# Kernel optimization log

Measured on AMD Instinct MI355X. Metric: run time of the kernel, lower is better.

The kernel has to match this reference:

```python
import jax, jax.numpy as jnp
import numpy as np

N_QUBITS = 8
N_LAYERS = 2


def _apply_1q(state, U, wire):
    # state: (B, 2, ..., 2) with N_QUBITS qubit axes; U: (2,2) complex, shared over batch
    s = jnp.moveaxis(state, 1 + wire, 1)
    shp = s.shape
    out = jnp.einsum('ij,bjr->bir', U, s.reshape(shp[0], 2, -1)).reshape(shp)
    return jnp.moveaxis(out, 1, 1 + wire)


def _apply_cnot(state, c, t):
    s = jnp.moveaxis(state, (1 + c, 1 + t), (1, 2))  # (B, ctrl, tgt, ...)
    s_new = jnp.stack([s[:, 0], jnp.flip(s[:, 1], axis=1)], axis=1)
    return jnp.moveaxis(s_new, (1, 2), (1 + c, 1 + t))


def _circuit(angles, q_weights):
    # angles: (B, N) real; q_weights: (L, N, 3) real
    B = angles.shape[0]
    N = N_QUBITS
    # AngleEmbedding with RY on |0...0> -> product state [cos(a/2), sin(a/2)] per qubit
    half = angles * 0.5
    state = jnp.ones((B, 1), dtype=jnp.complex64)
    for i in range(N):
        v = jnp.stack([jnp.cos(half[:, i]), jnp.sin(half[:, i])], axis=-1).astype(jnp.complex64)
        state = (state[:, :, None] * v[:, None, :]).reshape(B, -1)
    state = state.reshape((B,) + (2,) * N)
    # StronglyEntanglingLayers: per layer, Rot(phi,theta,omega) on each wire then CNOT ring
    L = q_weights.shape[0]
    for l in range(L):
        for i in range(N):
            phi = q_weights[l, i, 0]
            theta = q_weights[l, i, 1]
            omega = q_weights[l, i, 2]
            c = jnp.cos(theta * 0.5).astype(jnp.complex64)
            s_ = jnp.sin(theta * 0.5).astype(jnp.complex64)
            ep = jnp.exp(-0.5j * (phi + omega).astype(jnp.complex64))
            em = jnp.exp(-0.5j * (phi - omega).astype(jnp.complex64))
            # Rot = RZ(omega) RY(theta) RZ(phi)
            U = jnp.stack([jnp.stack([ep * c, -jnp.conj(em) * s_]),
                           jnp.stack([em * s_, jnp.conj(ep) * c])])
            state = _apply_1q(state, U, i)
        r = l % (N - 1) + 1  # default range pattern of StronglyEntanglingLayers
        for i in range(N):
            state = _apply_cnot(state, i, (i + r) % N)
    # <Z_i> = P(bit_i=0) - P(bit_i=1)
    probs = jnp.real(state * jnp.conj(state))
    zs = []
    for i in range(N):
        pm = jnp.moveaxis(probs, 1 + i, 1).reshape(B, 2, -1).sum(-1)
        zs.append(pm[:, 0] - pm[:, 1])
    return jnp.stack(zs, axis=-1)  # (B, N) real


def setup_inputs() -> dict:
    key = jax.random.key(0)
    k1, k2, k3, k4 = jax.random.split(key, 4)
    B = 32768
    pca_x = jax.random.normal(k1, (B, N_QUBITS), dtype=jnp.float32)
    q_weights = jax.random.uniform(k2, (N_LAYERS, N_QUBITS, 3), dtype=jnp.float32) * (2.0 * np.pi)
    W = jax.random.normal(k3, (N_QUBITS, 64), dtype=jnp.float32) * 0.35
    b = jax.random.normal(k4, (64,), dtype=jnp.float32) * 0.02
    gamma = jnp.ones((64,), dtype=jnp.float32)
    beta = jnp.zeros((64,), dtype=jnp.float32)
    return {"pca_x": pca_x, "q_weights": q_weights, "W": W, "b": b, "gamma": gamma, "beta": beta}


def reference(pca_x, q_weights, W, b, gamma, beta):
    angles = jax.nn.sigmoid(pca_x) * jnp.pi  # (B, 8)
    z = _circuit(angles, q_weights).astype(pca_x.dtype)  # (B, 8) PauliZ expvals
    h = z @ W + b  # (B, 64)
    mu = jnp.mean(h, axis=-1, keepdims=True)
    var = jnp.mean((h - mu) ** 2, axis=-1, keepdims=True)
    hn = (h - mu) / jnp.sqrt(var + 1e-5) * gamma + beta
    return jax.nn.gelu(hn, approximate=False)
```

## Files before the change

### kernel.cpp

```cpp
#include <hip/hip_runtime.h>
#include <math.h>

#define DEVFN __device__ __forceinline__

typedef __attribute__((ext_vector_type(8))) _Float16 f16x8;
typedef __attribute__((ext_vector_type(4))) float f32x4;

DEVFN float shxor(float v, int m) { return __shfl_xor(v, m, 64); }

template<int W>
DEVFN void rot_gate(int lane, float (&sr)[4], float (&si)[4], const float* u) {
  const float u00r=u[0], u00i=u[1], u01r=u[2], u01i=u[3];
  const float u10r=u[4], u10i=u[5], u11r=u[6], u11i=u[7];
  if constexpr (W <= 5) {
    constexpr int M = 1 << (5 - W);
    const bool hi = (lane & M) != 0;
    const float cmr = hi ? u11r : u00r, cmi = hi ? u11i : u00i;
    const float cor = hi ? u10r : u01r, coi = hi ? u10i : u01i;
    #pragma unroll
    for (int k = 0; k < 4; ++k) {
      float orr = shxor(sr[k], M);
      float oii = shxor(si[k], M);
      float nr = cmr*sr[k] - cmi*si[k] + cor*orr - coi*oii;
      float ni = cmr*si[k] + cmi*sr[k] + cor*oii + coi*orr;
      sr[k] = nr; si[k] = ni;
    }
  } else {
    constexpr int KB = (W == 6) ? 2 : 1;
    #pragma unroll
    for (int k0 = 0; k0 < 4; ++k0) {
      if ((k0 & KB) == 0) {
        const int k1 = k0 | KB;
        float ar = sr[k0], ai = si[k0];
        float br = sr[k1], bi = si[k1];
        sr[k0] = u00r*ar - u00i*ai + u01r*br - u01i*bi;
        si[k0] = u00r*ai + u00i*ar + u01r*bi + u01i*br;
        sr[k1] = u10r*ar - u10i*ai + u11r*br - u11i*bi;
        si[k1] = u10r*ai + u10i*ar + u11r*bi + u11i*br;
      }
    }
  }
}

template<int C, int T>
DEVFN void cnot_gate(int lane, float (&sr)[4], float (&si)[4]) {
  constexpr int PC = 7 - C, PT = 7 - T;
  if constexpr (PT >= 2) {
    constexpr int M = 1 << (PT - 2);
    #pragma unroll
    for (int k = 0; k < 4; ++k) {
      float orr = shxor(sr[k], M);
      float oii = shxor(si[k], M);
      bool ctrl;
      if constexpr (PC >= 2) ctrl = ((lane >> (PC - 2)) & 1) != 0;
      else                   ctrl = ((k >> PC) & 1) != 0;
      if (ctrl) { sr[k] = orr; si[k] = oii; }
    }
  } else {
    float tr[4], ti[4];
    #pragma unroll
    for (int k = 0; k < 4; ++k) { tr[k] = sr[k]; ti[k] = si[k]; }
    #pragma unroll
    for (int k = 0; k < 4; ++k) {
      bool ctrl;
      if constexpr (PC >= 2) ctrl = ((lane >> (PC - 2)) & 1) != 0;
      else                   ctrl = ((k >> PC) & 1) != 0;
      if (ctrl) { sr[k] = tr[k ^ (1 << PT)]; si[k] = ti[k ^ (1 << PT)]; }
    }
  }
}

__global__ __launch_bounds__(64) void qsb_prep(
    const float* __restrict__ qw, const float* __restrict__ Wm,
    const float* __restrict__ bias,
    _Float16* __restrict__ Bfrag, float* __restrict__ stats) {
  __shared__ float uL[16 * 8];
  int bid = blockIdx.x;
  int lane = threadIdx.x;
  if (bid < 256) {
    if (lane < 16) {
      int l = lane >> 3, i = lane & 7;
      float phi = qw[l*24 + i*3 + 0];
      float th  = qw[l*24 + i*3 + 1];
      float om  = qw[l*24 + i*3 + 2];
      float cth = cosf(0.5f*th), sth = sinf(0.5f*th);
      float ap = 0.5f*(phi+om), am = 0.5f*(phi-om);
      float cap = cosf(ap), sap = sinf(ap);
      float cam = cosf(am), sam = sinf(am);
      float* u = &uL[lane*8];
      u[0] =  cap*cth; u[1] = -sap*cth;
      u[2] = -cam*sth; u[3] = -sam*sth;
      u[4] =  cam*sth; u[5] = -sam*sth;
      u[6] =  cap*cth; u[7] =  sap*cth;
    }
    __syncthreads();
    int col = bid;
    float sr[4], si[4];
    #pragma unroll
    for (int k = 0; k < 4; ++k) { sr[k] = (lane*4 + k == col) ? 1.f : 0.f; si[k] = 0.f; }
    rot_gate<0>(lane, sr, si, &uL[0*8]);
    rot_gate<1>(lane, sr, si, &uL[1*8]);
    rot_gate<2>(lane, sr, si, &uL[2*8]);
    rot_gate<3>(lane, sr, si, &uL[3*8]);
    rot_gate<4>(lane, sr, si, &uL[4*8]);
    rot_gate<5>(lane, sr, si, &uL[5*8]);
    rot_gate<6>(lane, sr, si, &uL[6*8]);
    rot_gate<7>(lane, sr, si, &uL[7*8]);
    cnot_gate<0,1>(lane, sr, si);
    cnot_gate<1,2>(lane, sr, si);
    cnot_gate<2,3>(lane, sr, si);
    cnot_gate<3,4>(lane, sr, si);
    cnot_gate<4,5>(lane, sr, si);
    cnot_gate<5,6>(lane, sr, si);
    cnot_gate<6,7>(lane, sr, si);
    cnot_gate<7,0>(lane, sr, si);
    rot_gate<0>(lane, sr, si, &uL[(8+0)*8]);
    rot_gate<1>(lane, sr, si, &uL[(8+1)*8]);
    rot_gate<2>(lane, sr, si, &uL[(8+2)*8]);
    rot_gate<3>(lane, sr, si, &uL[(8+3)*8]);
    rot_gate<4>(lane, sr, si, &uL[(8+4)*8]);
    rot_gate<5>(lane, sr, si, &uL[(8+5)*8]);
    rot_gate<6>(lane, sr, si, &uL[(8+6)*8]);
    rot_gate<7>(lane, sr, si, &uL[(8+7)*8]);
    cnot_gate<0,2>(lane, sr, si);
    cnot_gate<1,3>(lane, sr, si);
    cnot_gate<2,4>(lane, sr, si);
    cnot_gate<3,5>(lane, sr, si);
    cnot_gate<4,6>(lane, sr, si);
    cnot_gate<5,7>(lane, sr, si);
    cnot_gate<6,0>(lane, sr, si);
    cnot_gate<7,1>(lane, sr, si);
    const int ks = col >> 5, kg = (col >> 3) & 3, e = col & 7;
    #pragma unroll
    for (int k = 0; k < 4; ++k) {
      int a = lane*4 + k;
      int ch = a >> 5, nf = (a >> 4) & 1, cf = a & 15;
      int pos = (kg*16 + cf)*8 + e;
      Bfrag[((ch*4 + nf    )*8 + ks)*512 + pos] = (_Float16)sr[k];
      Bfrag[((ch*4 + 2 + nf)*8 + ks)*512 + pos] = (_Float16)si[k];
    }
  } else {
    int t = lane;
    {
      int i = t >> 3, j = t & 7;
      float s = 0.f;
      for (int c = 0; c < 64; ++c) s += Wm[i*64 + c] * Wm[j*64 + c];
      stats[16 + t] = s * 0.015625f;
    }
    if (t < 8) {
      float s = 0.f, sb = 0.f;
      for (int c = 0; c < 64; ++c) { float w = Wm[t*64 + c]; s += w; sb += w * bias[c]; }
      stats[t]     = s * 0.015625f;
      stats[8 + t] = 2.f * sb * 0.015625f;
    }
    if (t == 0) {
      float s = 0.f, s2 = 0.f;
      for (int c = 0; c < 64; ++c) { s += bias[c]; s2 += bias[c]*bias[c]; }
      stats[80] = s * 0.015625f;
      stats[81] = s2 * 0.015625f;
    }
  }
}

__global__ __launch_bounds__(512, 4) void qsb_main(
    const float* __restrict__ pca, const _Float16* __restrict__ Bfrag,
    const float* __restrict__ statsG,
    const float* __restrict__ Wm, const float* __restrict__ bias,
    const float* __restrict__ gamma, const float* __restrict__ beta,
    float* __restrict__ out, int B) {
  __shared__ __align__(16) _Float16 A3[16384];
  __shared__ float zpart[64 * 49];
  __shared__ float zrow[64 * 8];
  __shared__ float musig[64 * 2];
  __shared__ float Wl[512];
  __shared__ float biasL[64], gammaL[64], betaL[64];
  __shared__ float statsL[82];

  const int tid = threadIdx.x;
  const int wid = tid >> 6, lane = tid & 63;
  const int r0 = blockIdx.x * 64;

  Wl[tid] = Wm[tid];
  if (tid < 64) { biasL[tid] = bias[tid]; gammaL[tid] = gamma[tid]; betaL[tid] = beta[tid]; }
  if (tid >= 64 && tid < 146) statsL[tid - 64] = statsG[tid - 64];

  {
    const int rl = tid >> 3, tq = tid & 7;
    const int r = r0 + rl;
    float cv[8], sv[8];
    #pragma unroll
    for (int w = 0; w < 8; ++w) { cv[w] = 1.f; sv[w] = 0.f; }
    if (r < B) {
      #pragma unroll
      for (int w = 0; w < 8; ++w) {
        float x = pca[r*8 + w];
        float sg = __builtin_amdgcn_rcpf(1.f + __expf(-x));
        float ang = 1.5707963267948966f * sg;
        cv[w] = __cosf(ang); sv[w] = __sinf(ang);
      }
    }
    float base = ((tq & 4) ? sv[0] : cv[0]) * ((tq & 2) ? sv[1] : cv[1])
               * ((tq & 1) ? sv[2] : cv[2]);
    float arr[32];
    arr[0] = base;
    #pragma unroll
    for (int p = 0; p < 5; ++p) {
      const int w = 7 - p;
      const int sz = 1 << p;
      #pragma unroll
      for (int i = 0; i < (1 << p); ++i) {
        arr[i + sz] = arr[i] * sv[w];
        arr[i]      = arr[i] * cv[w];
      }
    }
    _Float16* dstBase = &A3[((tq*4 + (rl >> 4))*16 + (rl & 15))*32];
    #pragma unroll
    for (int ib = 0; ib < 4; ++ib) {
      f16x8 v;
      #pragma unroll
      for (int j = 0; j < 8; ++j) v[j] = (_Float16)arr[ib*8 + j];
      *(f16x8*)(dstBase + (ib ^ (tq & 3))*8) = v;
    }
  }
  __syncthreads();

  const int cfrag = lane & 15, kgrp = lane >> 4;
  f32x4 acc[4][4];
  #pragma unroll
  for (int m = 0; m < 4; ++m)
    #pragma unroll
    for (int q = 0; q < 4; ++q) acc[m][q] = (f32x4){0.f, 0.f, 0.f, 0.f};

  const _Float16* Bw = Bfrag + (wid*4)*8*512 + lane*8;
  #pragma unroll 2
  for (int ks = 0; ks < 8; ++ks) {
    const int slot = (kgrp ^ (ks & 3))*8;
    f16x8 af[4];
    #pragma unroll
    for (int m = 0; m < 4; ++m)
      af[m] = *(const f16x8*)&A3[((ks*4 + m)*16 + cfrag)*32 + slot];
    #pragma unroll
    for (int q = 0; q < 4; ++q) {
      f16x8 bq = *(const f16x8*)(Bw + (q*8 + ks)*512);
      #pragma unroll
      for (int m = 0; m < 4; ++m)
        acc[m][q] = __builtin_amdgcn_mfma_f32_16x16x32_f16(af[m], bq, acc[m][q], 0, 0, 0);
    }
  }

  #pragma unroll
  for (int m = 0; m < 4; ++m) {
    #pragma unroll
    for (int j = 0; j < 4; ++j) {
      float re0 = acc[m][0][j], re1 = acc[m][1][j];
      float im0 = acc[m][2][j], im1 = acc[m][3][j];
      float p0 = re0*re0 + im0*im0;
      float p1 = re1*re1 + im1*im1;
      float T = p0 + p1, S4 = p0 - p1;
      #pragma unroll
      for (int mm = 1; mm < 16; mm <<= 1) {
        S4 += shxor(S4, mm);
        float t2 = shxor(T, mm);
        T = (lane & mm) ? (t2 - T) : (T + t2);
      }
      const int row = m*16 + kgrp*4 + j;
      float* zp = &zpart[row*49 + wid*6];
      const int cc = lane & 15;
      if      (cc == 0) { zp[0] = T; zp[1] = S4; }
      else if (cc == 8) zp[2] = T;
      else if (cc == 4) zp[3] = T;
      else if (cc == 2) zp[4] = T;
      else if (cc == 1) zp[5] = T;
    }
  }
  __syncthreads();

  {
    const int row = tid >> 3, wire = tid & 7;
    const float* zp = &zpart[row*49];
    const int slot = (wire < 3) ? 0 : (wire - 2);
    const int sm = (wire == 0) ? 4 : (wire == 1) ? 2 : (wire == 2) ? 1 : 0;
    float a = 0.f;
    #pragma unroll
    for (int ch = 0; ch < 8; ++ch) {
      float v = zp[ch*6 + slot];
      a += (ch & sm) ? -v : v;
    }
    zrow[row*8 + wire] = a;
  }
  __syncthreads();

  {
    const int row = tid >> 3, ii = tid & 7;
    float zj[8];
    #pragma unroll
    for (int j = 0; j < 8; ++j) zj[j] = zrow[row*8 + j];
    float qi = statsL[8 + ii];
    #pragma unroll
    for (int j = 0; j < 8; ++j) qi += statsL[16 + ii*8 + j] * zj[j];
    float e2p = zj[ii] * qi;
    float mup = statsL[ii] * zj[ii];
    e2p += shxor(e2p, 1); e2p += shxor(e2p, 2); e2p += shxor(e2p, 4);
    mup += shxor(mup, 1); mup += shxor(mup, 2); mup += shxor(mup, 4);
    if (ii == 0) {
      float mu = mup + statsL[80];
      float e2 = e2p + statsL[81];
      float var = e2 - mu*mu;
      musig[row*2]     = mu;
      musig[row*2 + 1] = rsqrtf(fmaxf(var, 0.f) + 1e-5f);
    }
  }
  __syncthreads();

  #pragma unroll
  for (int rr = 0; rr < 8; ++rr) {
    const int row = wid*8 + rr;
    const int gr = r0 + row;
    float h = biasL[lane];
    #pragma unroll
    for (int i = 0; i < 8; ++i) h = fmaf(zrow[row*8 + i], Wl[i*64 + lane], h);
    float hn = (h - musig[row*2]) * musig[row*2 + 1] * gammaL[lane] + betaL[lane];
    float ge = 0.5f * hn * (1.f + erff(hn * 0.70710678118654752f));
    if (gr < B) out[gr*64 + lane] = ge;
  }
}

extern "C" void kernel_launch(void* const* d_in, const int* in_sizes, int n_in,
                              void* d_out, int out_size, void* d_ws, size_t ws_size,
                              hipStream_t stream) {
  const float* pca   = (const float*)d_in[0];
  const float* qw    = (const float*)d_in[1];
  const float* Wm    = (const float*)d_in[2];
  const float* bias  = (const float*)d_in[3];
  const float* gamma = (const float*)d_in[4];
  const float* beta  = (const float*)d_in[5];
  float* out = (float*)d_out;

  _Float16* Bfrag = (_Float16*)d_ws;
  float* stats = (float*)((char*)d_ws + 512*256*2);

  int B = in_sizes[0] / 8;

  hipLaunchKernelGGL(qsb_prep, dim3(257), dim3(64), 0, stream, qw, Wm, bias, Bfrag, stats);
  int blocks = (B + 63) / 64;
  hipLaunchKernelGGL(qsb_main, dim3(blocks), dim3(512), 0, stream,
                     pca, Bfrag, stats, Wm, bias, gamma, beta, out, B);
}
```

Measured before the change: 31.42 us.

## Halve block size and reduce Pauli-Z probabilities with a sign-matrix MFMA

Blocks now cover 32 rows with 256 threads, and each wave handles two 16-wide chunks of the state. Per-chunk B fragments are double-buffered in registers so loads overlap the MFMAs. The shuffle-based butterfly that computed the Z expectation sums is replaced by writing squared amplitudes to LDS as fp16 and multiplying them by a constant ±1 sign fragment with one MFMA. The z-combine and stats stages are merged, and one block barrier is dropped because each wave only reads its own rows. This cuts shuffle and ALU work and raises occupancy, but rounding probabilities to fp16 before summing adds precision risk.

```diff
diff --git a/kernel.cpp b/kernel.cpp
--- a/kernel.cpp
+++ b/kernel.cpp
@@ -162,27 +162,47 @@
   }
 }
 
-__global__ __launch_bounds__(512, 4) void qsb_main(
+__global__ __launch_bounds__(256, 4) void qsb_main(
     const float* __restrict__ pca, const _Float16* __restrict__ Bfrag,
     const float* __restrict__ statsG,
     const float* __restrict__ Wm, const float* __restrict__ bias,
     const float* __restrict__ gamma, const float* __restrict__ beta,
     float* __restrict__ out, int B) {
-  __shared__ __align__(16) _Float16 A3[16384];
-  __shared__ float zpart[64 * 49];
-  __shared__ float zrow[64 * 8];
-  __shared__ float musig[64 * 2];
+  __shared__ __align__(16) _Float16 A3[8192];
+  __shared__ __align__(16) _Float16 YL[4 * 1280];
+  __shared__ float zpart[2304];
+  __shared__ float zrow[256];
+  __shared__ float musig[64];
   __shared__ float Wl[512];
   __shared__ float biasL[64], gammaL[64], betaL[64];
   __shared__ float statsL[82];
 
   const int tid = threadIdx.x;
   const int wid = tid >> 6, lane = tid & 63;
-  const int r0 = blockIdx.x * 64;
-
-  Wl[tid] = Wm[tid];
-  if (tid < 64) { biasL[tid] = bias[tid]; gammaL[tid] = gamma[tid]; betaL[tid] = beta[tid]; }
-  if (tid >= 64 && tid < 146) statsL[tid - 64] = statsG[tid - 64];
+  const int cfrag = lane & 15, kgrp = lane >> 4;
+  const int r0 = blockIdx.x * 32;
+
+  #pragma unroll
+  for (int i = tid; i < 512; i += 256) Wl[i] = Wm[i];
+  if (tid >= 256 - 64) {
+    int t = tid - (256 - 64);
+    biasL[t] = bias[t]; gammaL[t] = gamma[t]; betaL[t] = beta[t];
+  }
+  if (tid < 82) statsL[tid] = statsG[tid];
+
+  f16x8 sfrag;
+  #pragma unroll
+  for (int e = 0; e < 8; ++e) {
+    float v;
+    if      (cfrag == 0) v = 1.f;
+    else if (cfrag == 1) v = (kgrp & 2) ? -1.f : 1.f;
+    else if (cfrag == 2) v = (kgrp & 1) ? -1.f : 1.f;
+    else if (cfrag == 3) v = (e & 4)    ? -1.f : 1.f;
+    else if (cfrag == 4) v = (e & 2)    ? -1.f : 1.f;
+    else if (cfrag == 5) v = (e & 1)    ? -1.f : 1.f;
+    else v = 0.f;
+    sfrag[e] = (_Float16)v;
+  }
 
   {
     const int rl = tid >> 3, tq = tid & 7;
@@ -213,7 +233,7 @@
         arr[i]      = arr[i] * cv[w];
       }
     }
-    _Float16* dstBase = &A3[((tq*4 + (rl >> 4))*16 + (rl & 15))*32];
+    _Float16* dstBase = &A3[((tq*2 + (rl >> 4))*16 + (rl & 15))*32];
     #pragma unroll
     for (int ib = 0; ib < 4; ++ib) {
       f16x8 v;
@@ -224,85 +244,98 @@
   }
   __syncthreads();
 
-  const int cfrag = lane & 15, kgrp = lane >> 4;
-  f32x4 acc[4][4];
+  _Float16* Yw = &YL[wid * 1280];
   #pragma unroll
-  for (int m = 0; m < 4; ++m)
-    #pragma unroll
-    for (int q = 0; q < 4; ++q) acc[m][q] = (f32x4){0.f, 0.f, 0.f, 0.f};
-
-  const _Float16* Bw = Bfrag + (wid*4)*8*512 + lane*8;
-  #pragma unroll 2
-  for (int ks = 0; ks < 8; ++ks) {
-    const int slot = (kgrp ^ (ks & 3))*8;
-    f16x8 af[4];
-    #pragma unroll
-    for (int m = 0; m < 4; ++m)
-      af[m] = *(const f16x8*)&A3[((ks*4 + m)*16 + cfrag)*32 + slot];
-    #pragma unroll
-    for (int q = 0; q < 4; ++q) {
-      f16x8 bq = *(const f16x8*)(Bw + (q*8 + ks)*512);
-      #pragma unroll
-      for (int m = 0; m < 4; ++m)
-        acc[m][q] = __builtin_amdgcn_mfma_f32_16x16x32_f16(af[m], bq, acc[m][q], 0, 0, 0);
-    }
-  }
-
-  #pragma unroll
-  for (int m = 0; m < 4; ++m) {
-    #pragma unroll
-    for (int j = 0; j < 4; ++j) {
-      float re0 = acc[m][0][j], re1 = acc[m][1][j];
-      float im0 = acc[m][2][j], im1 = acc[m][3][j];
-      float p0 = re0*re0 + im0*im0;
-      float p1 = re1*re1 + im1*im1;
-      float T = p0 + p1, S4 = p0 - p1;
-      #pragma unroll
-      for (int mm = 1; mm < 16; mm <<= 1) {
-        S4 += shxor(S4, mm);
-        float t2 = shxor(T, mm);
-        T = (lane & mm) ? (t2 - T) : (T + t2);
-      }
-      const int row = m*16 + kgrp*4 + j;
-      float* zp = &zpart[row*49 + wid*6];
-      const int cc = lane & 15;
-      if      (cc == 0) { zp[0] = T; zp[1] = S4; }
-      else if (cc == 8) zp[2] = T;
-      else if (cc == 4) zp[3] = T;
-      else if (cc == 2) zp[4] = T;
-      else if (cc == 1) zp[5] = T;
+  for (int c = 0; c < 2; ++c) {
+    const int ch = wid*2 + c;
+    const _Float16* Bw = Bfrag + (size_t)(ch*4)*8*512 + lane*8;
+
+    f32x4 acc[2][4];
+    #pragma unroll
+    for (int m = 0; m < 2; ++m)
+      #pragma unroll
+      for (int q = 0; q < 4; ++q) acc[m][q] = (f32x4){0.f, 0.f, 0.f, 0.f};
+
+    f16x8 bqA[4], bqB[4];
+    #pragma unroll
+    for (int q = 0; q < 4; ++q) bqA[q] = *(const f16x8*)(Bw + (q*8 + 0)*512);
+
+    #pragma unroll
+    for (int kp = 0; kp < 4; ++kp) {
+      const int ks0 = kp*2, ks1 = kp*2 + 1;
+      #pragma unroll
+      for (int q = 0; q < 4; ++q) bqB[q] = *(const f16x8*)(Bw + (q*8 + ks1)*512);
+      {
+        f16x8 af0 = *(const f16x8*)&A3[((ks0*2 + 0)*16 + cfrag)*32 + (kgrp ^ (ks0 & 3))*8];
+        f16x8 af1 = *(const f16x8*)&A3[((ks0*2 + 1)*16 + cfrag)*32 + (kgrp ^ (ks0 & 3))*8];
+        #pragma unroll
+        for (int q = 0; q < 4; ++q) {
+          acc[0][q] = __builtin_amdgcn_mfma_f32_16x16x32_f16(af0, bqA[q], acc[0][q], 0, 0, 0);
+          acc[1][q] = __builtin_amdgcn_mfma_f32_16x16x32_f16(af1, bqA[q], acc[1][q], 0, 0, 0);
+        }
+      }
+      if (kp < 3) {
+        #pragma unroll
+        for (int q = 0; q < 4; ++q) bqA[q] = *(const f16x8*)(Bw + (q*8 + ks0 + 2)*512);
+      }
+      {
+        f16x8 af0 = *(const f16x8*)&A3[((ks1*2 + 0)*16 + cfrag)*32 + (kgrp ^ (ks1 & 3))*8];
+        f16x8 af1 = *(const f16x8*)&A3[((ks1*2 + 1)*16 + cfrag)*32 + (kgrp ^ (ks1 & 3))*8];
+        #pragma unroll
+        for (int q = 0; q < 4; ++q) {
+          acc[0][q] = __builtin_amdgcn_mfma_f32_16x16x32_f16(af0, bqB[q], acc[0][q], 0, 0, 0);
+          acc[1][q] = __builtin_amdgcn_mfma_f32_16x16x32_f16(af1, bqB[q], acc[1][q], 0, 0, 0);
+        }
+      }
+    }
+
+    #pragma unroll
+    for (int m = 0; m < 2; ++m) {
+      #pragma unroll
+      for (int nf = 0; nf < 2; ++nf) {
+        #pragma unroll
+        for (int j = 0; j < 4; ++j) {
+          float re = acc[m][nf][j], im = acc[m][2 + nf][j];
+          float p = re*re + im*im;
+          Yw[m*640 + (kgrp*4 + j)*40 + nf*16 + cfrag] = (_Float16)p;
+        }
+      }
+    }
+    #pragma unroll
+    for (int m = 0; m < 2; ++m) {
+      f16x8 yfrag = *(const f16x8*)&Yw[m*640 + (lane & 15)*40 + kgrp*8];
+      f32x4 d = __builtin_amdgcn_mfma_f32_16x16x32_f16(yfrag, sfrag, (f32x4){0.f,0.f,0.f,0.f}, 0, 0, 0);
+      if (cfrag < 6) {
+        #pragma unroll
+        for (int j = 0; j < 4; ++j)
+          zpart[(ch*32 + m*16 + kgrp*4 + j)*9 + cfrag] = d[j];
+      }
     }
   }
   __syncthreads();
 
   {
-    const int row = tid >> 3, wire = tid & 7;
-    const float* zp = &zpart[row*49];
-    const int slot = (wire < 3) ? 0 : (wire - 2);
-    const int sm = (wire == 0) ? 4 : (wire == 1) ? 2 : (wire == 2) ? 1 : 0;
-    float a = 0.f;
+    const int row = tid >> 3, w = tid & 7;
+    const int slot = (w < 3) ? 0 : (w - 2);
+    const int sm = (w == 0) ? 4 : (w == 1) ? 2 : (w == 2) ? 1 : 0;
+    float z = 0.f;
     #pragma unroll
     for (int ch = 0; ch < 8; ++ch) {
-      float v = zp[ch*6 + slot];
-      a += (ch & sm) ? -v : v;
-    }
-    zrow[row*8 + wire] = a;
-  }
-  __syncthreads();
-
-  {
-    const int row = tid >> 3, ii = tid & 7;
-    float zj[8];
-    #pragma unroll
-    for (int j = 0; j < 8; ++j) zj[j] = zrow[row*8 + j];
-    float qi = statsL[8 + ii];
-    #pragma unroll
-    for (int j = 0; j < 8; ++j) qi += statsL[16 + ii*8 + j] * zj[j];
-    float e2p = zj[ii] * qi;
-    float mup = statsL[ii] * zj[ii];
+      float v = zpart[(ch*32 + row)*9 + slot];
+      z += (ch & sm) ? -v : v;
+    }
+    zrow[row*8 + w] = z;
+    f32x4 zlo = *(const f32x4*)&zrow[row*8];
+    f32x4 zhi = *(const f32x4*)&zrow[row*8 + 4];
+    float zj[8] = {zlo[0], zlo[1], zlo[2], zlo[3], zhi[0], zhi[1], zhi[2], zhi[3]};
+    float qi = statsL[8 + w];
+    #pragma unroll
+    for (int j = 0; j < 8; ++j) qi += statsL[16 + w*8 + j] * zj[j];
+    float e2p = zj[w] * qi;
+    float mup = statsL[w] * zj[w];
     e2p += shxor(e2p, 1); e2p += shxor(e2p, 2); e2p += shxor(e2p, 4);
     mup += shxor(mup, 1); mup += shxor(mup, 2); mup += shxor(mup, 4);
-    if (ii == 0) {
+    if (w == 0) {
       float mu = mup + statsL[80];
       float e2 = e2p + statsL[81];
       float var = e2 - mu*mu;
@@ -310,7 +343,6 @@
       musig[row*2 + 1] = rsqrtf(fmaxf(var, 0.f) + 1e-5f);
     }
   }
-  __syncthreads();
 
   #pragma unroll
   for (int rr = 0; rr < 8; ++rr) {
@@ -342,7 +374,7 @@
   int B = in_sizes[0] / 8;
 
   hipLaunchKernelGGL(qsb_prep, dim3(257), dim3(64), 0, stream, qw, Wm, bias, Bfrag, stats);
-  int blocks = (B + 63) / 64;
-  hipLaunchKernelGGL(qsb_main, dim3(blocks), dim3(512), 0, stream,
+  int blocks = (B + 31) / 32;
+  hipLaunchKernelGGL(qsb_main, dim3(blocks), dim3(256), 0, stream,
                      pca, Bfrag, stats, Wm, bias, gamma, beta, out, B);
 }
```

Result: faster. 28.58 us (-9.0%).
